# Kernel tuning notes

Hardware: AMD Instinct MI355X
Metric: run time of the kernel (lower is better)

The kernel has to match this reference:

```python
import jax, jax.numpy as jnp
import numpy as np
from jax import lax


def conv2d(x, w, b, stride, pad):
    # x: NCHW, w: OIHW (PyTorch Conv2d layout)
    y = lax.conv_general_dilated(x, w, (stride, stride), ((pad, pad), (pad, pad)),
                                 dimension_numbers=('NCHW', 'OIHW', 'NCHW'))
    return y + b[None, :, None, None]


def conv_transpose2d(x, w, b, stride, pad):
    # PyTorch ConvTranspose2d weight layout: (in_ch, out_ch, kH, kW).
    # Equivalent to a conv with lhs dilation, flipped kernel, in/out swapped.
    k = w.shape[2]
    w2 = jnp.transpose(jnp.flip(w, (2, 3)), (1, 0, 2, 3))  # (out, in, k, k)
    p = k - 1 - pad
    y = lax.conv_general_dilated(x, w2, (1, 1), ((p, p), (p, p)),
                                 lhs_dilation=(stride, stride),
                                 dimension_numbers=('NCHW', 'OIHW', 'NCHW'))
    return y + b[None, :, None, None]


def setup_inputs() -> dict:
    key = jax.random.key(0)
    ks = jax.random.split(key, 8)
    K, D = 512, 64  # num_embeddings, embedding_dim
    x = jax.random.uniform(ks[0], (32, 3, 256, 256), jnp.float32)

    def he(k, shape, fan_in):
        return jax.random.normal(k, shape, jnp.float32) * np.float32(np.sqrt(2.0 / fan_in))

    w1 = he(ks[1], (64, 3, 4, 4), 3 * 16);   b1 = jnp.zeros((64,), jnp.float32)
    w2 = he(ks[2], (D, 64, 4, 4), 64 * 16);  b2 = jnp.zeros((D,), jnp.float32)
    # codebook init: uniform(-1/K, 1/K) as in the torch module
    codebook = jax.random.uniform(ks[3], (K, D), jnp.float32, -1.0 / K, 1.0 / K)
    dw1 = he(ks[4], (D, 64, 4, 4), D * 16);  db1 = jnp.zeros((64,), jnp.float32)
    dw2 = he(ks[5], (64, 3, 4, 4), 64 * 16); db2 = jnp.zeros((3,), jnp.float32)
    return dict(x=x, w1=w1, b1=b1, w2=w2, b2=b2, codebook=codebook,
                dw1=dw1, db1=db1, dw2=dw2, db2=db2)


def reference(x, w1, b1, w2, b2, codebook, dw1, db1, dw2, db2):
    # Encoder
    z_e = jax.nn.relu(conv2d(x, w1, b1, 2, 1))
    z_e = jax.nn.relu(conv2d(z_e, w2, b2, 2, 1))  # (N, D, H/4, W/4)
    D = z_e.shape[1]
    # Faithful to torch: .view(-1, C) on contiguous NCHW (NO channel permute)
    zf = z_e.reshape(-1, D)  # (N*Hq*Wq, D) given D == Hq here numerically; rows are contiguous slices
    # ||z - e||^2 = ||z||^2 + ||e||^2 - 2 z.e  -> (M, K) distance matrix
    d = (jnp.sum(zf * zf, axis=1, keepdims=True)
         + jnp.sum(codebook * codebook, axis=1)
         - 2.0 * (zf @ codebook.T))
    idx = jnp.argmin(d, axis=1)           # (M,) int
    z_q = codebook[idx].reshape(z_e.shape)  # gather + reshape back to z_e shape
    # Decoder
    h = jax.nn.relu(conv_transpose2d(z_q, dw1, db1, 2, 1))
    x_recon = jax.nn.sigmoid(conv_transpose2d(h, dw2, db2, 2, 1))
    return x_recon, z_q
```

## Files before the change

### kernel.cpp

```cpp
#include <hip/hip_runtime.h>
#include <math.h>


typedef __attribute__((ext_vector_type(8))) short short8;
typedef __attribute__((ext_vector_type(4))) short short4v;
typedef __attribute__((ext_vector_type(4))) float f32x4;

#define MFMA16(a, b, c) __builtin_amdgcn_mfma_f32_16x16x32_bf16((a), (b), (c), 0, 0, 0)

__device__ __forceinline__ short f2bf(float f) {
  union { float f; unsigned u; } x; x.f = f;
  unsigned r = (x.u + 0x7FFFu + ((x.u >> 16) & 1u)) >> 16;
  return (short)r;
}
__device__ __forceinline__ float bf2f(short s) {
  union { unsigned u; float f; } x;
  x.u = ((unsigned)(unsigned short)s) << 16;
  return x.f;
}

__global__ __launch_bounds__(256) void k_prep(const float* __restrict__ w2,
                                              const float* __restrict__ dw1,
                                              const float* __restrict__ dw2,
                                              const float* __restrict__ cb,
                                              short* __restrict__ A2,
                                              short* __restrict__ AD1,
                                              short* __restrict__ AD2,
                                              short* __restrict__ cbb,
                                              float* __restrict__ cnm) {
  int i = blockIdx.x * 256 + threadIdx.x;
  {
    int t = i >> 12, oc = (i >> 6) & 63, c = i & 63;
    A2[i] = f2bf(w2[(oc * 64 + c) * 16 + t]);
  }
  {
    int p = i >> 14, ab = (i >> 12) & 3, oc = (i >> 6) & 63, c = i & 63;
    int kh = 1 - (p >> 1) + 2 * (ab >> 1);
    int kw = 1 - (p & 1) + 2 * (ab & 1);
    AD1[i] = f2bf(dw1[(c * 64 + oc) * 16 + kh * 4 + kw]);
  }
  if (i < 16384) {
    int p = i >> 12, ab = (i >> 10) & 3, oc = (i >> 6) & 15, c = i & 63;
    int kh = 1 - (p >> 1) + 2 * (ab >> 1);
    int kw = 1 - (p & 1) + 2 * (ab & 1);
    short v = 0;
    if (oc < 3) v = f2bf(dw2[(c * 3 + oc) * 16 + kh * 4 + kw]);
    AD2[i] = v;
  }
  if (i < 32768) cbb[i] = f2bf(cb[i]);
  if (i < 512) {
    float s = 0.f;
    for (int d = 0; d < 64; ++d) { float v = cb[i * 64 + d]; s += v * v; }
    cnm[i] = s;
  }
}

__global__ __launch_bounds__(256) void k_conv1(const float* __restrict__ x,
                                               const float* __restrict__ w1,
                                               const float* __restrict__ b1,
                                               short* __restrict__ z1T) {
  __shared__ float sW[3 * 16 * 64];
  __shared__ float sB[64];
  __shared__ float sIn[3 * 34 * 34];
  __shared__ short sOutC[256 * 72];
  const int tid = threadIdx.x;

  for (int i = tid; i < 3072; i += 256) {
    int oc = i & 63, t = (i >> 6) & 15, c = i >> 10;
    sW[i] = w1[(oc * 3 + c) * 16 + t];
  }
  if (tid < 64) sB[tid] = b1[tid];

  const int b = blockIdx.x;
  const int n = b >> 6;
  const int tile = b & 63;
  const int tr = tile >> 3, tc = tile & 7;
  const int oh0 = tr * 16, ow0 = tc * 16;
  const int ih_base = oh0 * 2 - 1, iw_base = ow0 * 2 - 1;

  for (int i = tid; i < 3468; i += 256) {
    int c = i / 1156;
    int rem = i - c * 1156;
    int r = rem / 34;
    int col = rem - r * 34;
    int ih = ih_base + r, iw = iw_base + col;
    float v = 0.f;
    if ((unsigned)ih < 256u && (unsigned)iw < 256u)
      v = x[((n * 3 + c) * 256 + ih) * 256 + iw];
    sIn[i] = v;
  }
  __syncthreads();

  const int ty = tid >> 4, tx = tid & 15;
  float acc[64];
#pragma unroll
  for (int j = 0; j < 64; ++j) acc[j] = sB[j];

  for (int c = 0; c < 3; ++c) {
    for (int t = 0; t < 16; ++t) {
      int kh = t >> 2, kw = t & 3;
      float v = sIn[c * 1156 + (2 * ty + kh) * 34 + (2 * tx + kw)];
      const float4* wp = (const float4*)&sW[(c * 16 + t) * 64];
#pragma unroll
      for (int j = 0; j < 16; ++j) {
        float4 w4 = wp[j];
        acc[4 * j + 0] += v * w4.x;
        acc[4 * j + 1] += v * w4.y;
        acc[4 * j + 2] += v * w4.z;
        acc[4 * j + 3] += v * w4.w;
      }
    }
  }

  const int sp = ty * 16 + tx;
#pragma unroll
  for (int kk = 0; kk < 8; ++kk) {
    short8 v;
#pragma unroll
    for (int t2 = 0; t2 < 8; ++t2) {
      float r = acc[8 * kk + t2];
      v[t2] = f2bf(r > 0.f ? r : 0.f);
    }
    *(short8*)&sOutC[sp * 72 + 8 * kk] = v;
  }
  __syncthreads();
  const int r = tid >> 4, jj = tid & 15;
#pragma unroll
  for (int it = 0; it < 8; ++it) {
    int chunk = jj + 16 * it;
    int owL = chunk >> 3, c8 = chunk & 7;
    short8 v = *(const short8*)&sOutC[(r * 16 + owL) * 72 + 8 * c8];
    *(short8*)(z1T + (((long)(n * 128 + oh0 + r) * 128) + ow0 + owL) * 64 + 8 * c8) = v;
  }
}

__global__ __launch_bounds__(256) void k_conv2(const short* __restrict__ z1T,
                                               const short* __restrict__ A2,
                                               const float* __restrict__ b2,
                                               short* __restrict__ ze) {
  __shared__ char smemC[62400];
  __shared__ float sB2c[64];
  short* slab = (short*)smemC;
  short* sOut = (short*)smemC;

  const int tid = threadIdx.x;
  if (tid < 64) sB2c[tid] = b2[tid];
  const int b = blockIdx.x;
  const int n = b >> 5;
  const int oh0 = (b & 31) * 2;
  const int w = tid >> 6, l = tid & 63;
  const int row = w >> 1, mh = w & 1;
  const int e = l & 15, kg = l >> 4;
  const int ih0 = 2 * oh0 - 1;

  f32x4 acc[2][4];
#pragma unroll
  for (int mi = 0; mi < 2; ++mi)
#pragma unroll
    for (int nt = 0; nt < 4; ++nt) acc[mi][nt] = (f32x4){0.f, 0.f, 0.f, 0.f};

  for (int p = 0; p < 2; ++p) {
    const int c0 = 32 * p;
    __syncthreads();
    for (int i = tid; i < 3120; i += 256) {
      int r = i / 520;
      int rem = i - r * 520;
      int iwL = rem >> 2, li = rem & 3;
      int ih = ih0 + r, iw = iwL - 1;
      short8 v = {0, 0, 0, 0, 0, 0, 0, 0};
      if ((unsigned)ih < 128u && (unsigned)iw < 128u)
        v = *(const short8*)(z1T + (((long)(n * 128 + ih) * 128) + iw) * 64 + c0 + 8 * li);
      *(short8*)&slab[8 * ((r * 130 + iwL) * 5 + li)] = v;
    }
    __syncthreads();

    for (int t = 0; t < 16; ++t) {
      const int kh = t >> 2, kw = t & 3;
      const int rL = 2 * row + kh;
      short8 aF[2], bF[4];
#pragma unroll
      for (int mi = 0; mi < 2; ++mi)
        aF[mi] = *(const short8*)(A2 + ((t * 64 + 32 * mh + 16 * mi + e) * 64) + c0 + 8 * kg);
#pragma unroll
      for (int nt = 0; nt < 4; ++nt) {
        int iwL = 2 * (nt * 16 + e) + kw;
        bF[nt] = *(const short8*)&slab[8 * ((rL * 130 + iwL) * 5 + kg)];
      }
#pragma unroll
      for (int mi = 0; mi < 2; ++mi)
#pragma unroll
        for (int nt = 0; nt < 4; ++nt)
          acc[mi][nt] = MFMA16(aF[mi], bF[nt], acc[mi][nt]);
    }
  }

  __syncthreads();
#pragma unroll
  for (int mi = 0; mi < 2; ++mi)
#pragma unroll
    for (int nt = 0; nt < 4; ++nt)
#pragma unroll
      for (int rr = 0; rr < 4; ++rr) {
        int oc = 32 * mh + 16 * mi + 4 * kg + rr;
        float v = acc[mi][nt][rr] + sB2c[oc];
        sOut[(row * 64 + oc) * 68 + nt * 16 + e] = f2bf(v > 0.f ? v : 0.f);
      }
  __syncthreads();
  {
    int oc = 32 * mh + (l >> 1);
    int half = l & 1;
#pragma unroll
    for (int j = 0; j < 8; ++j) {
      short4v v = *(const short4v*)&sOut[(row * 64 + oc) * 68 + 32 * half + 4 * j];
      *(short4v*)(ze + (((long)(n * 64 + oc) * 64) + oh0 + row) * 64 + 32 * half + 4 * j) = v;
    }
  }
}

__global__ __launch_bounds__(256) void k_vq(const short* __restrict__ zeb,
                                            const short* __restrict__ cbb,
                                            const float* __restrict__ cnm,
                                            const float* __restrict__ cb,
                                            float* __restrict__ zq,
                                            short* __restrict__ zqT) {
  const int tid = threadIdx.x;
  const int wv = tid >> 6, l = tid & 63;
  const int e = l & 15, kg = l >> 4;
  const int b = blockIdx.x;
  const int n = b >> 6, h = b & 63;

  const short* zebase = zeb + (((long)(n * 64 + 16 * wv + e) * 64) + h) * 64;
  short8 aF0 = *(const short8*)(zebase + 8 * kg);
  short8 aF1 = *(const short8*)(zebase + 32 + 8 * kg);

  float bestD[4];
  int bestI[4];
#pragma unroll
  for (int rr = 0; rr < 4; ++rr) { bestD[rr] = 3.4e38f; bestI[rr] = 0; }

  for (int ch = 0; ch < 8; ++ch) {
    f32x4 acc[4];
#pragma unroll
    for (int nt = 0; nt < 4; ++nt) {
      acc[nt] = (f32x4){0.f, 0.f, 0.f, 0.f};
      const short* cbase = cbb + (ch * 64 + nt * 16 + e) * 64;
      short8 b0 = *(const short8*)(cbase + 8 * kg);
      short8 b1 = *(const short8*)(cbase + 32 + 8 * kg);
      acc[nt] = MFMA16(aF0, b0, acc[nt]);
      acc[nt] = MFMA16(aF1, b1, acc[nt]);
    }
#pragma unroll
    for (int nt = 0; nt < 4; ++nt) {
      int code = ch * 64 + nt * 16 + e;
      float cn = cnm[code];
#pragma unroll
      for (int rr = 0; rr < 4; ++rr) {
        float d = cn - 2.f * acc[nt][rr];
        if (d < bestD[rr]) { bestD[rr] = d; bestI[rr] = code; }
      }
    }
  }
#pragma unroll
  for (int m = 1; m <= 8; m <<= 1) {
#pragma unroll
    for (int rr = 0; rr < 4; ++rr) {
      float od = __shfl_xor(bestD[rr], m);
      int oi = __shfl_xor(bestI[rr], m);
      if (od < bestD[rr] || (od == bestD[rr] && oi < bestI[rr])) {
        bestD[rr] = od; bestI[rr] = oi;
      }
    }
  }
#pragma unroll
  for (int rr = 0; rr < 4; ++rr) {
    int c = 16 * wv + 4 * kg + rr;
    int idx = bestI[rr];
    float4 v = *(const float4*)(cb + idx * 64 + 4 * e);
    *(float4*)(zq + (((long)(n * 64 + c) * 64) + h) * 64 + 4 * e) = v;
    short* qt = zqT + (((long)(n * 64 + h) * 64) + 4 * e) * 64 + c;
    qt[0] = f2bf(v.x);
    qt[64] = f2bf(v.y);
    qt[128] = f2bf(v.z);
    qt[192] = f2bf(v.w);
  }
}

__global__ __launch_bounds__(256) void k_deconv1(const short* __restrict__ zqT,
                                                 const short* __restrict__ AD1,
                                                 const float* __restrict__ db1,
                                                 short* __restrict__ hT) {
  __shared__ char smemD[34816];
  __shared__ float sBias[64];
  short* slab = (short*)smemD;
  short* sOut = (short*)smemD;

  const int tid = threadIdx.x;
  if (tid < 64) sBias[tid] = db1[tid];
  const int b = blockIdx.x;
  const int n = b >> 6, i0 = b & 63;
  const int w = tid >> 6, l = tid & 63;
  const int ph = w >> 1, pw = w & 1;
  const int e = l & 15, kg = l >> 4;

  for (int i = tid; i < 1584; i += 256) {
    int r = i / 528;
    int rem = i - r * 528;
    int iwL = rem >> 3, li = rem & 7;
    int ih = i0 - 1 + r, iw = iwL - 1;
    short8 v = {0, 0, 0, 0, 0, 0, 0, 0};
    if ((unsigned)ih < 64u && (unsigned)iw < 64u)
      v = *(const short8*)(zqT + (((long)(n * 64 + ih) * 64) + iw) * 64 + 8 * li);
    *(short8*)&slab[(r * 66 + iwL) * 72 + 8 * li] = v;
  }
  __syncthreads();

  f32x4 acc[4][4];
#pragma unroll
  for (int m = 0; m < 4; ++m)
#pragma unroll
    for (int nt = 0; nt < 4; ++nt) acc[m][nt] = (f32x4){0.f, 0.f, 0.f, 0.f};

  for (int ab = 0; ab < 4; ++ab) {
    const int rL = 1 + ph - (ab >> 1);
    const int coff = pw - (ab & 1) + 1;
#pragma unroll
    for (int ks = 0; ks < 2; ++ks) {
      short8 aF[4], bF[4];
#pragma unroll
      for (int m = 0; m < 4; ++m)
        aF[m] = *(const short8*)(AD1 + (((w * 4 + ab) * 64 + 16 * m + e) * 64) + 32 * ks + 8 * kg);
#pragma unroll
      for (int nt = 0; nt < 4; ++nt) {
        int iwL = nt * 16 + e + coff;
        bF[nt] = *(const short8*)&slab[(rL * 66 + iwL) * 72 + 32 * ks + 8 * kg];
      }
#pragma unroll
      for (int m = 0; m < 4; ++m)
#pragma unroll
        for (int nt = 0; nt < 4; ++nt)
          acc[m][nt] = MFMA16(aF[m], bF[nt], acc[m][nt]);
    }
  }

  __syncthreads();
#pragma unroll
  for (int m = 0; m < 4; ++m)
#pragma unroll
    for (int nt = 0; nt < 4; ++nt) {
      int owIdx = nt * 16 + e;
      int oc0 = 16 * m + 4 * kg;
      short4v o;
#pragma unroll
      for (int rr = 0; rr < 4; ++rr) {
        float v = acc[m][nt][rr] + sBias[oc0 + rr];
        o[rr] = f2bf(v > 0.f ? v : 0.f);
      }
      *(short4v*)&sOut[((w * 64 + owIdx) * 68) + oc0] = o;
    }
  __syncthreads();
  {
    const int oh = 2 * i0 + ph;
    const int ow = 2 * l + pw;
    short* dst = hT + (((long)(n * 128 + oh) * 128) + ow) * 64;
#pragma unroll
    for (int j = 0; j < 16; ++j) {
      short4v v = *(const short4v*)&sOut[((w * 64 + l) * 68) + 4 * j];
      *(short4v*)(dst + 4 * j) = v;
    }
  }
}

__global__ __launch_bounds__(256) void k_deconv2(const short* __restrict__ hT,
                                                 const short* __restrict__ AD2,
                                                 const float* __restrict__ db2,
                                                 float* __restrict__ xr) {
  __shared__ char smemE[53856];
  __shared__ float sB2[3];
  short* sIn = (short*)smemE;
  float* sOut = (float*)smemE;

  const int tid = threadIdx.x;
  if (tid < 3) sB2[tid] = db2[tid];
  const int b = blockIdx.x;
  const int n = b >> 6;
  const int rem0 = b & 63;
  const int q = rem0 >> 1, wh = rem0 & 1;
  const int w = tid >> 6, l = tid & 63;
  const int ph = w >> 1, pw = w & 1;
  const int e = l & 15, kg = l >> 4;

  for (int i = tid; i < 3168; i += 256) {
    int r = i / 528;
    int rr2 = i - r * 528;
    int iwL = rr2 >> 3, li = rr2 & 7;
    int ih = 4 * q - 1 + r, iw = 64 * wh - 1 + iwL;
    short8 v = {0, 0, 0, 0, 0, 0, 0, 0};
    if ((unsigned)ih < 128u && (unsigned)iw < 128u)
      v = *(const short8*)(hT + (((long)(n * 128 + ih) * 128) + iw) * 64 + 8 * li);
    *(short8*)&sIn[(r * 66 + iwL) * 68 + 8 * li] = v;
  }

  short8 aF[8];
#pragma unroll
  for (int ab = 0; ab < 4; ++ab)
#pragma unroll
    for (int chh = 0; chh < 2; ++chh)
      aF[ab * 2 + chh] = *(const short8*)(AD2 + (((w * 4 + ab) * 16 + e) * 64) + 32 * chh + 8 * kg);

  __syncthreads();

  f32x4 acc[4][4];
#pragma unroll
  for (int j = 0; j < 4; ++j)
#pragma unroll
    for (int nt = 0; nt < 4; ++nt) acc[j][nt] = (f32x4){0.f, 0.f, 0.f, 0.f};

  const int colBase = e + pw + 1;
  const int rowBase = 1 + ph;

#pragma unroll
  for (int ab = 0; ab < 4; ++ab) {
    const int a = ab >> 1, bb = ab & 1;
#pragma unroll
    for (int chh = 0; chh < 2; ++chh) {
      short8 af = aF[ab * 2 + chh];
#pragma unroll
      for (int j = 0; j < 4; ++j) {
        const int rL = rowBase + j - a;
#pragma unroll
        for (int nt = 0; nt < 4; ++nt) {
          const int iwL = nt * 16 + colBase - bb;
          short8 bf = *(const short8*)&sIn[(rL * 66 + iwL) * 68 + 32 * chh + 8 * kg];
          acc[j][nt] = MFMA16(af, bf, acc[j][nt]);
        }
      }
    }
  }

  __syncthreads();
  if (kg == 0) {
#pragma unroll
    for (int j = 0; j < 4; ++j)
#pragma unroll
      for (int nt = 0; nt < 4; ++nt) {
        int ohl = 2 * j + ph;
        int owl = 2 * (nt * 16 + e) + pw;
#pragma unroll
        for (int rr = 0; rr < 3; ++rr) {
          float v = 1.f / (1.f + expf(-(acc[j][nt][rr] + sB2[rr])));
          sOut[(rr * 8 + ohl) * 128 + owl] = v;
        }
      }
  }
  __syncthreads();
  for (int i = tid; i < 768; i += 256) {
    int oc = i >> 8, r2 = i & 255;
    int ohl = r2 >> 5, c4 = r2 & 31;
    float4 v = ((const float4*)sOut)[i];
    *(float4*)(xr + (((long)(n * 3 + oc) * 256) + 8 * q + ohl) * 256 + 128 * wh + 4 * c4) = v;
  }
}

extern "C" void kernel_launch(void* const* d_in, const int* in_sizes, int n_in,
                              void* d_out, int out_size, void* d_ws, size_t ws_size,
                              hipStream_t stream) {
  (void)in_sizes; (void)n_in; (void)out_size; (void)ws_size;

  const float* x   = (const float*)d_in[0];
  const float* w1  = (const float*)d_in[1];
  const float* b1  = (const float*)d_in[2];
  const float* w2  = (const float*)d_in[3];
  const float* b2  = (const float*)d_in[4];
  const float* cb  = (const float*)d_in[5];
  const float* dw1 = (const float*)d_in[6];
  const float* db1 = (const float*)d_in[7];
  const float* dw2 = (const float*)d_in[8];
  const float* db2 = (const float*)d_in[9];

  char* wsb = (char*)d_ws;
  short* z1T = (short*)wsb;
  short* zeb = (short*)(wsb + 67108864);
  short* zqT = (short*)(wsb + 83886080);
  short* A2  = (short*)(wsb + 100663296);
  short* AD1 = (short*)(wsb + 100794368);
  short* cbb = (short*)(wsb + 100925440);
  float* cnm = (float*)(wsb + 100990976);
  short* AD2 = (short*)(wsb + 100993024);
  short* hT  = z1T;

  float* xr = (float*)d_out;
  float* zq = (float*)d_out + 6291456;

  k_prep<<<256, 256, 0, stream>>>(w2, dw1, dw2, cb, A2, AD1, AD2, cbb, cnm);
  k_conv1<<<2048, 256, 0, stream>>>(x, w1, b1, z1T);
  k_conv2<<<1024, 256, 0, stream>>>(z1T, A2, b2, zeb);
  k_vq<<<2048, 256, 0, stream>>>(zeb, cbb, cnm, cb, zq, zqT);
  k_deconv1<<<2048, 256, 0, stream>>>(zqT, AD1, db1, hT);
  k_deconv2<<<2048, 256, 0, stream>>>(hT, AD2, db2, xr);
}
```

Baseline: 503.5 us.

## Batch global loads into registers before LDS stores; split deconv2 channels into double-buffered halves

The shared-memory staging loops in conv1, conv2 and deconv1 are unrolled so every global load is issued into registers before any LDS store, which lets more loads be in flight at once. deconv2 is reorganised: each block covers half as many output rows (twice the grid), and its 64 input channels are staged in two 32-channel halves. The second half's global loads are issued before the MFMAs on the first half run, overlapping memory with compute. The smaller LDS footprint may raise occupancy, at the cost of more registers and more halo reloads across the larger grid.

```diff
diff --git a/kernel.cpp b/kernel.cpp
--- a/kernel.cpp
+++ b/kernel.cpp
@@ -65,9 +65,16 @@
   __shared__ short sOutC[256 * 72];
   const int tid = threadIdx.x;
 
-  for (int i = tid; i < 3072; i += 256) {
-    int oc = i & 63, t = (i >> 6) & 15, c = i >> 10;
-    sW[i] = w1[(oc * 3 + c) * 16 + t];
+  {
+    float tw[12];
+#pragma unroll
+    for (int it = 0; it < 12; ++it) {
+      int i = tid + 256 * it;
+      int oc = i & 63, t = (i >> 6) & 15, c = i >> 10;
+      tw[it] = w1[(oc * 3 + c) * 16 + t];
+    }
+#pragma unroll
+    for (int it = 0; it < 12; ++it) sW[tid + 256 * it] = tw[it];
   }
   if (tid < 64) sB[tid] = b1[tid];
 
@@ -78,16 +85,26 @@
   const int oh0 = tr * 16, ow0 = tc * 16;
   const int ih_base = oh0 * 2 - 1, iw_base = ow0 * 2 - 1;
 
-  for (int i = tid; i < 3468; i += 256) {
-    int c = i / 1156;
-    int rem = i - c * 1156;
-    int r = rem / 34;
-    int col = rem - r * 34;
-    int ih = ih_base + r, iw = iw_base + col;
-    float v = 0.f;
-    if ((unsigned)ih < 256u && (unsigned)iw < 256u)
-      v = x[((n * 3 + c) * 256 + ih) * 256 + iw];
-    sIn[i] = v;
+  {
+    float t[14]; bool vd[14];
+#pragma unroll
+    for (int it = 0; it < 14; ++it) {
+      int i = tid + 256 * it;
+      vd[it] = i < 3468;
+      int ii = vd[it] ? i : 0;
+      int c = ii / 1156;
+      int rem = ii - c * 1156;
+      int r = rem / 34;
+      int col = rem - r * 34;
+      int ih = ih_base + r, iw = iw_base + col;
+      float v = 0.f;
+      if (vd[it] && (unsigned)ih < 256u && (unsigned)iw < 256u)
+        v = x[((n * 3 + c) * 256 + ih) * 256 + iw];
+      t[it] = v;
+    }
+#pragma unroll
+    for (int it = 0; it < 14; ++it)
+      if (vd[it]) sIn[tid + 256 * it] = t[it];
   }
   __syncthreads();
 
@@ -162,15 +179,44 @@
   for (int p = 0; p < 2; ++p) {
     const int c0 = 32 * p;
     __syncthreads();
-    for (int i = tid; i < 3120; i += 256) {
-      int r = i / 520;
-      int rem = i - r * 520;
-      int iwL = rem >> 2, li = rem & 3;
-      int ih = ih0 + r, iw = iwL - 1;
-      short8 v = {0, 0, 0, 0, 0, 0, 0, 0};
-      if ((unsigned)ih < 128u && (unsigned)iw < 128u)
-        v = *(const short8*)(z1T + (((long)(n * 128 + ih) * 128) + iw) * 64 + c0 + 8 * li);
-      *(short8*)&slab[8 * ((r * 130 + iwL) * 5 + li)] = v;
+    {
+      short8 ta[7]; int off[7];
+#pragma unroll
+      for (int it = 0; it < 7; ++it) {
+        int i = tid + 256 * it;
+        int r = i / 520;
+        int rem = i - r * 520;
+        int iwL = rem >> 2, li = rem & 3;
+        int ih = ih0 + r, iw = iwL - 1;
+        off[it] = 8 * ((r * 130 + iwL) * 5 + li);
+        short8 v = {0, 0, 0, 0, 0, 0, 0, 0};
+        if ((unsigned)ih < 128u && (unsigned)iw < 128u)
+          v = *(const short8*)(z1T + (((long)(n * 128 + ih) * 128) + iw) * 64 + c0 + 8 * li);
+        ta[it] = v;
+      }
+#pragma unroll
+      for (int it = 0; it < 7; ++it) *(short8*)&slab[off[it]] = ta[it];
+    }
+    {
+      short8 tb[6]; int off[6]; bool vd[6];
+#pragma unroll
+      for (int it = 0; it < 6; ++it) {
+        int i = tid + 256 * (7 + it);
+        vd[it] = i < 3120;
+        int ii = vd[it] ? i : 0;
+        int r = ii / 520;
+        int rem = ii - r * 520;
+        int iwL = rem >> 2, li = rem & 3;
+        int ih = ih0 + r, iw = iwL - 1;
+        off[it] = 8 * ((r * 130 + iwL) * 5 + li);
+        short8 v = {0, 0, 0, 0, 0, 0, 0, 0};
+        if (vd[it] && (unsigned)ih < 128u && (unsigned)iw < 128u)
+          v = *(const short8*)(z1T + (((long)(n * 128 + ih) * 128) + iw) * 64 + c0 + 8 * li);
+        tb[it] = v;
+      }
+#pragma unroll
+      for (int it = 0; it < 6; ++it)
+        if (vd[it]) *(short8*)&slab[off[it]] = tb[it];
     }
     __syncthreads();
 
@@ -302,15 +348,26 @@
   const int ph = w >> 1, pw = w & 1;
   const int e = l & 15, kg = l >> 4;
 
-  for (int i = tid; i < 1584; i += 256) {
-    int r = i / 528;
-    int rem = i - r * 528;
-    int iwL = rem >> 3, li = rem & 7;
-    int ih = i0 - 1 + r, iw = iwL - 1;
-    short8 v = {0, 0, 0, 0, 0, 0, 0, 0};
-    if ((unsigned)ih < 64u && (unsigned)iw < 64u)
-      v = *(const short8*)(zqT + (((long)(n * 64 + ih) * 64) + iw) * 64 + 8 * li);
-    *(short8*)&slab[(r * 66 + iwL) * 72 + 8 * li] = v;
+  {
+    short8 t[7]; int off[7]; bool vd[7];
+#pragma unroll
+    for (int it = 0; it < 7; ++it) {
+      int i = tid + 256 * it;
+      vd[it] = i < 1584;
+      int ii = vd[it] ? i : 0;
+      int r = ii / 528;
+      int rem = ii - r * 528;
+      int iwL = rem >> 3, li = rem & 7;
+      int ih = i0 - 1 + r, iw = iwL - 1;
+      off[it] = (r * 66 + iwL) * 72 + 8 * li;
+      short8 v = {0, 0, 0, 0, 0, 0, 0, 0};
+      if (vd[it] && (unsigned)ih < 64u && (unsigned)iw < 64u)
+        v = *(const short8*)(zqT + (((long)(n * 64 + ih) * 64) + iw) * 64 + 8 * li);
+      t[it] = v;
+    }
+#pragma unroll
+    for (int it = 0; it < 7; ++it)
+      if (vd[it]) *(short8*)&slab[off[it]] = t[it];
   }
   __syncthreads();
 
@@ -374,73 +431,115 @@
                                                  const short* __restrict__ AD2,
                                                  const float* __restrict__ db2,
                                                  float* __restrict__ xr) {
-  __shared__ char smemE[53856];
+  __shared__ __align__(16) char smem[38016];
   __shared__ float sB2[3];
-  short* sIn = (short*)smemE;
-  float* sOut = (float*)smemE;
+  short* buf0 = (short*)smem;
+  short* buf1 = (short*)(smem + 19008);
+  float* sOut = (float*)smem;
 
   const int tid = threadIdx.x;
   if (tid < 3) sB2[tid] = db2[tid];
   const int b = blockIdx.x;
-  const int n = b >> 6;
-  const int rem0 = b & 63;
+  const int n = b >> 7;
+  const int rem0 = b & 127;
   const int q = rem0 >> 1, wh = rem0 & 1;
   const int w = tid >> 6, l = tid & 63;
   const int ph = w >> 1, pw = w & 1;
   const int e = l & 15, kg = l >> 4;
 
-  for (int i = tid; i < 3168; i += 256) {
-    int r = i / 528;
-    int rr2 = i - r * 528;
-    int iwL = rr2 >> 3, li = rr2 & 7;
-    int ih = 4 * q - 1 + r, iw = 64 * wh - 1 + iwL;
+  int soff[5]; long sga[5]; bool sv[5], sin[5];
+#pragma unroll
+  for (int it = 0; it < 5; ++it) {
+    int i = tid + 256 * it;
+    sv[it] = i < 1056;
+    int ii = sv[it] ? i : 0;
+    int r = ii / 264;
+    int rm = ii - r * 264;
+    int iwL = rm >> 2, li = rm & 3;
+    int ih = 2 * q - 1 + r, iw = 64 * wh - 1 + iwL;
+    sin[it] = sv[it] && (unsigned)ih < 128u && (unsigned)iw < 128u;
+    soff[it] = (r * 66 + iwL) * 36 + 8 * li;
+    sga[it] = (((long)(n * 128 + ih) * 128) + iw) * 64 + 8 * li;
+  }
+
+  {
+    short8 t0[5];
+#pragma unroll
+    for (int it = 0; it < 5; ++it) {
+      short8 v = {0, 0, 0, 0, 0, 0, 0, 0};
+      if (sin[it]) v = *(const short8*)(hT + sga[it]);
+      t0[it] = v;
+    }
+#pragma unroll
+    for (int it = 0; it < 5; ++it)
+      if (sv[it]) *(short8*)&buf0[soff[it]] = t0[it];
+  }
+  __syncthreads();
+
+  short8 t1[5];
+#pragma unroll
+  for (int it = 0; it < 5; ++it) {
     short8 v = {0, 0, 0, 0, 0, 0, 0, 0};
-    if ((unsigned)ih < 128u && (unsigned)iw < 128u)
-      v = *(const short8*)(hT + (((long)(n * 128 + ih) * 128) + iw) * 64 + 8 * li);
-    *(short8*)&sIn[(r * 66 + iwL) * 68 + 8 * li] = v;
-  }
-
-  short8 aF[8];
-#pragma unroll
-  for (int ab = 0; ab < 4; ++ab)
-#pragma unroll
-    for (int chh = 0; chh < 2; ++chh)
-      aF[ab * 2 + chh] = *(const short8*)(AD2 + (((w * 4 + ab) * 16 + e) * 64) + 32 * chh + 8 * kg);
-
-  __syncthreads();
-
-  f32x4 acc[4][4];
-#pragma unroll
-  for (int j = 0; j < 4; ++j)
+    if (sin[it]) v = *(const short8*)(hT + sga[it] + 32);
+    t1[it] = v;
+  }
+
+  f32x4 acc[2][4];
+#pragma unroll
+  for (int j = 0; j < 2; ++j)
 #pragma unroll
     for (int nt = 0; nt < 4; ++nt) acc[j][nt] = (f32x4){0.f, 0.f, 0.f, 0.f};
 
-  const int colBase = e + pw + 1;
-  const int rowBase = 1 + ph;
-
-#pragma unroll
-  for (int ab = 0; ab < 4; ++ab) {
-    const int a = ab >> 1, bb = ab & 1;
-#pragma unroll
-    for (int chh = 0; chh < 2; ++chh) {
-      short8 af = aF[ab * 2 + chh];
-#pragma unroll
-      for (int j = 0; j < 4; ++j) {
-        const int rL = rowBase + j - a;
+  {
+    short8 aF[4];
+#pragma unroll
+    for (int ab = 0; ab < 4; ++ab)
+      aF[ab] = *(const short8*)(AD2 + (((w * 4 + ab) * 16 + e) * 64) + 8 * kg);
+#pragma unroll
+    for (int ab = 0; ab < 4; ++ab) {
+      const int a = ab >> 1, bb = ab & 1;
+#pragma unroll
+      for (int j = 0; j < 2; ++j) {
+        const int rL = 1 + ph + j - a;
 #pragma unroll
         for (int nt = 0; nt < 4; ++nt) {
-          const int iwL = nt * 16 + colBase - bb;
-          short8 bf = *(const short8*)&sIn[(rL * 66 + iwL) * 68 + 32 * chh + 8 * kg];
-          acc[j][nt] = MFMA16(af, bf, acc[j][nt]);
+          const int iwL = nt * 16 + e + pw - bb + 1;
+          short8 bf = *(const short8*)&buf0[(rL * 66 + iwL) * 36 + 8 * kg];
+          acc[j][nt] = MFMA16(aF[ab], bf, acc[j][nt]);
         }
       }
     }
   }
 
-  __syncthreads();
+#pragma unroll
+  for (int it = 0; it < 5; ++it)
+    if (sv[it]) *(short8*)&buf1[soff[it]] = t1[it];
+  __syncthreads();
+
+  {
+    short8 aF[4];
+#pragma unroll
+    for (int ab = 0; ab < 4; ++ab)
+      aF[ab] = *(const short8*)(AD2 + (((w * 4 + ab) * 16 + e) * 64) + 32 + 8 * kg);
+#pragma unroll
+    for (int ab = 0; ab < 4; ++ab) {
+      const int a = ab >> 1, bb = ab & 1;
+#pragma unroll
+      for (int j = 0; j < 2; ++j) {
+        const int rL = 1 + ph + j - a;
+#pragma unroll
+        for (int nt = 0; nt < 4; ++nt) {
+          const int iwL = nt * 16 + e + pw - bb + 1;
+          short8 bf = *(const short8*)&buf1[(rL * 66 + iwL) * 36 + 8 * kg];
+          acc[j][nt] = MFMA16(aF[ab], bf, acc[j][nt]);
+        }
+      }
+    }
+  }
+
   if (kg == 0) {
 #pragma unroll
-    for (int j = 0; j < 4; ++j)
+    for (int j = 0; j < 2; ++j)
 #pragma unroll
       for (int nt = 0; nt < 4; ++nt) {
         int ohl = 2 * j + ph;
@@ -448,16 +547,20 @@
 #pragma unroll
         for (int rr = 0; rr < 3; ++rr) {
           float v = 1.f / (1.f + expf(-(acc[j][nt][rr] + sB2[rr])));
-          sOut[(rr * 8 + ohl) * 128 + owl] = v;
+          sOut[(rr * 4 + ohl) * 128 + owl] = v;
         }
       }
   }
   __syncthreads();
-  for (int i = tid; i < 768; i += 256) {
-    int oc = i >> 8, r2 = i & 255;
-    int ohl = r2 >> 5, c4 = r2 & 31;
-    float4 v = ((const float4*)sOut)[i];
-    *(float4*)(xr + (((long)(n * 3 + oc) * 256) + 8 * q + ohl) * 256 + 128 * wh + 4 * c4) = v;
+#pragma unroll
+  for (int it = 0; it < 2; ++it) {
+    int i = tid + 256 * it;
+    if (i < 384) {
+      int oc = i >> 7, r2 = i & 127;
+      int ohl = r2 >> 5, c4 = r2 & 31;
+      float4 v = ((const float4*)sOut)[i];
+      *(float4*)(xr + (((long)(n * 3 + oc) * 256) + 4 * q + ohl) * 256 + 128 * wh + 4 * c4) = v;
+    }
   }
 }
 
@@ -496,5 +599,5 @@
   k_conv2<<<1024, 256, 0, stream>>>(z1T, A2, b2, zeb);
   k_vq<<<2048, 256, 0, stream>>>(zeb, cbb, cnm, cb, zq, zqT);
   k_deconv1<<<2048, 256, 0, stream>>>(zqT, AD1, db1, hT);
-  k_deconv2<<<2048, 256, 0, stream>>>(hT, AD2, db2, xr);
-}
+  k_deconv2<<<4096, 256, 0, stream>>>(hT, AD2, db2, xr);
+}
```

Result: faster. 458.2 us (-9.0%).
